# Kernel tuning notes

Hardware: AMD Instinct MI355X
Metric: run time of the kernel (lower is better)

The kernel has to match this reference:

```python
import jax, jax.numpy as jnp
import numpy as np

N_NODES = 40000
N_EDGES = 640000
IN_F = 128
HID = 128
MAX_ITERS = 8  # torch loop runs MAX_ITERS + 1 state updates (epsilon=None)


def setup_inputs() -> dict:
    key = jax.random.key(0)
    k1, k2, k3, k4, k5, k6 = jax.random.split(key, 6)
    x = jax.random.normal(k1, (N_NODES, IN_F), dtype=jnp.float32)
    edge_index = jax.random.randint(k2, (2, N_EDGES), 0, N_NODES, dtype=jnp.int64)
    scale = 0.1 / np.sqrt(HID)  # keep tanh out of deep saturation (ESN-style spectral scaling)
    w_in0 = jax.random.normal(k3, (HID, IN_F), dtype=jnp.float32) * scale   # layer 0 input_weight
    w_rec0 = jax.random.normal(k4, (HID, HID), dtype=jnp.float32) * scale   # layer 0 recurrent_weight
    w_in1 = jax.random.normal(k5, (HID, HID), dtype=jnp.float32) * scale    # layer 1 input_weight
    w_rec1 = jax.random.normal(k6, (HID, HID), dtype=jnp.float32) * scale   # layer 1 recurrent_weight
    return {"edge_index": edge_index, "x": x,
            "w_in0": w_in0, "w_rec0": w_rec0, "w_in1": w_in1, "w_rec1": w_rec1}


def _embed(x_proj, w_rec, src, dst):
    # Fixed-point iteration: state = tanh(x_proj + aggr(state) @ w_rec)
    # aggr = sum of source-node states scattered to destination nodes (PyG aggr='add').
    state0 = jnp.zeros_like(x_proj)

    def step(state, _):
        aggr = jax.ops.segment_sum(state[src], dst, num_segments=N_NODES)  # [N, H]
        new_state = jnp.tanh(x_proj + aggr @ w_rec)
        return new_state, None

    state, _ = jax.lax.scan(step, state0, None, length=MAX_ITERS + 1)
    return state


def reference(edge_index, x, w_in0, w_rec0, w_in1, w_rec1):
    src, dst = edge_index[0], edge_index[1]
    h0 = _embed(x @ w_in0.T, w_rec0, src, dst)    # layer 0 embeddings [N, H]
    h1 = _embed(h0 @ w_in1.T, w_rec1, src, dst)   # layer 1 embeddings [N, H]
    return h1  # fully=False, pooling=None -> final layer node embeddings
```

## Files before the change

### kernel.cpp

```cpp
#include <hip/hip_runtime.h>
#include <math.h>

#define N_NODES 40000
#define N_EDGES 640000
#define HID 128
#define MAXW 64
#define ITERS 8
#define NH (N_NODES * HID)
#define NPB 16
#define FBLK (N_NODES / NPB)
#define DSTRIDE 32

typedef __bf16 bf16x8 __attribute__((ext_vector_type(8)));
typedef __bf16 bf16x4 __attribute__((ext_vector_type(4)));
typedef float floatx4 __attribute__((ext_vector_type(4)));

__global__ __launch_bounds__(256) void init_kernel(int* __restrict__ ell,
                                                   int* __restrict__ degp,
                                                   __bf16* __restrict__ padA,
                                                   __bf16* __restrict__ padB) {
    int i = blockIdx.x * 256 + threadIdx.x;
    int4 pad = {N_NODES, N_NODES, N_NODES, N_NODES};
    ((int4*)ell)[i] = pad;
    if (i < N_NODES * DSTRIDE / 4) {
        int4 z = {0, 0, 0, 0};
        ((int4*)degp)[i] = z;
    }
    if (i < HID / 8) {
        bf16x8 z;
#pragma unroll
        for (int j = 0; j < 8; ++j) z[j] = (__bf16)0.f;
        ((bf16x8*)padA)[i] = z;
        ((bf16x8*)padB)[i] = z;
    }
}

__global__ __launch_bounds__(256) void build_ell_kernel(const int* __restrict__ ei,
                                                        int* __restrict__ degp,
                                                        int* __restrict__ ell) {
    int e = blockIdx.x * 256 + threadIdx.x;
    if (e >= N_EDGES) return;
    int s = ei[e];
    int d = ei[N_EDGES + e];
    int c = atomicAdd(&degp[d * DSTRIDE], 1);
    if (c < MAXW) ell[d * MAXW + c] = s;
}

__global__ __launch_bounds__(256) void compact_deg_kernel(const int* __restrict__ degp,
                                                          int* __restrict__ deg) {
    int i = blockIdx.x * 256 + threadIdx.x;
    if (i >= N_NODES) return;
    int d = degp[i * DSTRIDE];
    deg[i] = d > MAXW ? MAXW : d;
}

__global__ __launch_bounds__(256) void pack_w_kernel(const float* __restrict__ w,
                                                     __bf16* __restrict__ pk, int trans) {
    int f = blockIdx.x * 256 + threadIdx.x;
    int j = f & 7, l = (f >> 3) & 63, t = (f >> 9) & 7, c = f >> 12;
    int k = c * 32 + (l >> 4) * 8 + j;
    int n = t * 16 + (l & 15);
    float v = trans ? w[n * HID + k] : w[k * HID + n];
    pk[f] = (__bf16)v;
}

__global__ __launch_bounds__(256) void cast_bf16_kernel(const float* __restrict__ x,
                                                        __bf16* __restrict__ o) {
    int i = blockIdx.x * 256 + threadIdx.x;
    float4 v = ((const float4*)x)[i];
    bf16x4 b;
    b[0] = (__bf16)v.x; b[1] = (__bf16)v.y; b[2] = (__bf16)v.z; b[3] = (__bf16)v.w;
    ((bf16x4*)o)[i] = b;
}

__global__ __launch_bounds__(256) void mfma_gemm_kernel(const __bf16* A,
                                                        const __bf16* __restrict__ Bpk,
                                                        __bf16* __restrict__ xp_bf,
                                                        __bf16* st_bf) {
    __shared__ float tile[4][16][132];
    int tid = threadIdx.x;
    int wv = tid >> 6, lane = tid & 63;
    int q = lane >> 4, cl = lane & 15;

    int row_a = blockIdx.x * 64 + wv * 16 + cl;
    bf16x8 a[4];
#pragma unroll
    for (int c = 0; c < 4; ++c)
        a[c] = *(const bf16x8*)(A + (size_t)row_a * HID + c * 32 + q * 8);

#pragma unroll
    for (int t = 0; t < 8; ++t) {
        floatx4 acc_t = {0.f, 0.f, 0.f, 0.f};
#pragma unroll
        for (int c = 0; c < 4; ++c) {
            bf16x8 b = *(const bf16x8*)(Bpk + (((c * 8 + t) * 64 + lane) << 3));
            acc_t = __builtin_amdgcn_mfma_f32_16x16x32_bf16(a[c], b, acc_t, 0, 0, 0);
        }
#pragma unroll
        for (int r = 0; r < 4; ++r)
            tile[wv][q * 4 + r][t * 16 + cl] = acc_t[r];
    }
    int row = lane >> 2, seg = lane & 3;
    size_t goff = (size_t)(blockIdx.x * 64 + wv * 16 + row) * HID + seg * 32;
    float v[32];
#pragma unroll
    for (int j = 0; j < 8; ++j) {
        floatx4 t4 = *(floatx4*)&tile[wv][row][seg * 32 + j * 4];
        v[j * 4] = t4[0]; v[j * 4 + 1] = t4[1]; v[j * 4 + 2] = t4[2]; v[j * 4 + 3] = t4[3];
    }
#pragma unroll
    for (int j = 0; j < 4; ++j) {
        bf16x8 o;
#pragma unroll
        for (int k = 0; k < 8; ++k) o[k] = (__bf16)v[j * 8 + k];
        *(bf16x8*)(xp_bf + goff + j * 8) = o;
    }
#pragma unroll
    for (int i = 0; i < 32; ++i) v[i] = tanhf(v[i]);
#pragma unroll
    for (int j = 0; j < 4; ++j) {
        bf16x8 o;
#pragma unroll
        for (int k = 0; k < 8; ++k) o[k] = (__bf16)v[j * 8 + k];
        *(bf16x8*)(st_bf + goff + j * 8) = o;
    }
}

__global__ __launch_bounds__(256, 8) void fused_iter_kernel(
    const __bf16* __restrict__ state_in,
    __bf16* __restrict__ state_out,
    const int* __restrict__ ell,
    const int* __restrict__ deg,
    const __bf16* __restrict__ Bpk,
    const __bf16* __restrict__ xproj,
    float* __restrict__ st_f32) {
    __shared__ __align__(16) char smem[8704];
    int(*ell_lds)[68] = (int(*)[68])smem;
    __bf16(*aggr_lds)[136] = (__bf16(*)[136])(smem + 4352);
    float(*tile)[132] = (float(*)[132])smem;

    int tid = threadIdx.x;
    int wv = tid >> 6, lane = tid & 63;
    int q = lane >> 4, f = lane & 15;
    int nb = blockIdx.x * NPB;

    int degv = deg[nb + (lane & 15)];
    int bmx = degv;
#pragma unroll
    for (int m = 1; m <= 8; m <<= 1) {
        int o = __shfl_xor(bmx, m);
        bmx = o > bmx ? o : bmx;
    }
    int nslots = (bmx + 3) & ~3;

    {
        int n = tid & 15, g = tid >> 4;
        if (g * 4 < nslots)
            *(int4*)&ell_lds[n][g * 4] = *(const int4*)&ell[(size_t)(nb + n) * MAXW + g * 4];
    }
    __syncthreads();

    int n = wv * 4 + q;
    int cn = __shfl(degv, n);
    int steps = (cn + 3) >> 2;
    float acc[8];
#pragma unroll
    for (int j = 0; j < 8; ++j) acc[j] = 0.f;
    for (int s = 0; s < steps; ++s) {
        int b0 = s * 4;
        int idx[4];
#pragma unroll
        for (int u = 0; u < 4; ++u) idx[u] = ell_lds[n][b0 + u];
        bf16x8 v[4];
#pragma unroll
        for (int u = 0; u < 4; ++u)
            v[u] = *(const bf16x8*)(state_in + (size_t)idx[u] * HID + f * 8);
#pragma unroll
        for (int j = 0; j < 8; ++j)
            acc[j] += ((float)v[0][j] + (float)v[1][j]) + ((float)v[2][j] + (float)v[3][j]);
    }
    {
        bf16x8 o;
#pragma unroll
        for (int j = 0; j < 8; ++j) o[j] = (__bf16)acc[j];
        *(bf16x8*)&aggr_lds[n][f * 8] = o;
    }
    __syncthreads();

    bf16x8 a[4];
#pragma unroll
    for (int c = 0; c < 4; ++c)
        a[c] = *(const bf16x8*)&aggr_lds[f][c * 32 + q * 8];
    __syncthreads();

#pragma unroll
    for (int tl = 0; tl < 2; ++tl) {
        int t = wv * 2 + tl;
        floatx4 acc_t = {0.f, 0.f, 0.f, 0.f};
#pragma unroll
        for (int c = 0; c < 4; ++c) {
            bf16x8 b = *(const bf16x8*)(Bpk + (((c * 8 + t) * 64 + lane) << 3));
            acc_t = __builtin_amdgcn_mfma_f32_16x16x32_bf16(a[c], b, acc_t, 0, 0, 0);
        }
#pragma unroll
        for (int r = 0; r < 4; ++r)
            tile[q * 4 + r][t * 16 + f] = acc_t[r];
    }

    int row = lane >> 2, seg = lane & 3;
    size_t goff = (size_t)(nb + row) * HID + wv * 32 + seg * 8;
    int lcol = wv * 32 + seg * 8;
    float v[8];
    bf16x8 bx = *(const bf16x8*)(xproj + goff);
#pragma unroll
    for (int j = 0; j < 2; ++j) {
        floatx4 t4 = *(floatx4*)&tile[row][lcol + j * 4];
        v[j * 4] = t4[0]; v[j * 4 + 1] = t4[1]; v[j * 4 + 2] = t4[2]; v[j * 4 + 3] = t4[3];
    }
#pragma unroll
    for (int k = 0; k < 8; ++k) v[k] = tanhf(v[k] + (float)bx[k]);
    {
        bf16x8 o;
#pragma unroll
        for (int k = 0; k < 8; ++k) o[k] = (__bf16)v[k];
        *(bf16x8*)(state_out + goff) = o;
    }
    if (st_f32) {
#pragma unroll
        for (int j = 0; j < 2; ++j) {
            float4 o = {v[j * 4], v[j * 4 + 1], v[j * 4 + 2], v[j * 4 + 3]};
            *(float4*)(st_f32 + goff + j * 4) = o;
        }
    }
}

extern "C" void kernel_launch(void* const* d_in, const int* in_sizes, int n_in,
                              void* d_out, int out_size, void* d_ws, size_t ws_size,
                              hipStream_t stream) {
    const int* ei = (const int*)d_in[0];
    const float* x = (const float*)d_in[1];
    const float* w_in0 = (const float*)d_in[2];
    const float* w_rec0 = (const float*)d_in[3];
    const float* w_in1 = (const float*)d_in[4];
    const float* w_rec1 = (const float*)d_in[5];
    float* out = (float*)d_out;

    __bf16* xproj_bf = (__bf16*)d_ws;
    __bf16* stateA = xproj_bf + NH;
    __bf16* stateB = stateA + NH + HID;
    __bf16* packs = stateB + NH + HID;
    int* deg = (int*)(packs + 4 * 16384);
    int* degp = deg + N_NODES;
    int* ell = degp + N_NODES * DSTRIDE;
    __bf16* pk_in0 = packs;
    __bf16* pk_rec0 = packs + 16384;
    __bf16* pk_in1 = packs + 2 * 16384;
    __bf16* pk_rec1 = packs + 3 * 16384;

    init_kernel<<<N_EDGES / 256, 256, 0, stream>>>(ell, degp, stateA + NH, stateB + NH);
    build_ell_kernel<<<N_EDGES / 256, 256, 0, stream>>>(ei, degp, ell);
    compact_deg_kernel<<<(N_NODES + 255) / 256, 256, 0, stream>>>(degp, deg);
    pack_w_kernel<<<64, 256, 0, stream>>>(w_in0, pk_in0, 1);
    pack_w_kernel<<<64, 256, 0, stream>>>(w_rec0, pk_rec0, 0);
    pack_w_kernel<<<64, 256, 0, stream>>>(w_in1, pk_in1, 1);
    pack_w_kernel<<<64, 256, 0, stream>>>(w_rec1, pk_rec1, 0);
    cast_bf16_kernel<<<NH / 4 / 256, 256, 0, stream>>>(x, stateB);

    for (int layer = 0; layer < 2; ++layer) {
        const __bf16* pk_in = layer ? pk_in1 : pk_in0;
        const __bf16* pk_rec = layer ? pk_rec1 : pk_rec0;
        const __bf16* xin = layer ? stateA : stateB;
        mfma_gemm_kernel<<<625, 256, 0, stream>>>(xin, pk_in, xproj_bf, stateA);
        for (int it = 0; it < ITERS; ++it) {
            const __bf16* sin = (it & 1) ? stateB : stateA;
            __bf16* sout = (it & 1) ? stateA : stateB;
            float* f32out = (layer == 1 && it == ITERS - 1) ? out : nullptr;
            fused_iter_kernel<<<FBLK, 256, 0, stream>>>(sin, sout, ell, deg,
                                                        pk_rec, xproj_bf, f32out);
        }
    }
}
```

Baseline: 540.6 us.

## Store node state in feature-sliced layout and gather slice by slice

Node state moves from row-major [N,128] to four 32-feature slices, each [N+1,32] with its own zero pad row. The gather loop walks one slice at a time, with four lanes per node covering different neighbours, then reduces across lanes with shuffles. The aim is to shrink the gathered working set per pass so it stays cache-resident, at the cost of extra shuffles and four passes over the neighbour list. Nontemporal loads and stores are added for the ELL indices, xproj and the outputs, and a __syncthreads is added before the tile readback in both kernels.

```diff
diff --git a/kernel.cpp b/kernel.cpp
--- a/kernel.cpp
+++ b/kernel.cpp
@@ -10,10 +10,16 @@
 #define NPB 16
 #define FBLK (N_NODES / NPB)
 #define DSTRIDE 32
+#define NN1 (N_NODES + 1)
+#define SLICES 4
+#define SW 32
 
 typedef __bf16 bf16x8 __attribute__((ext_vector_type(8)));
 typedef __bf16 bf16x4 __attribute__((ext_vector_type(4)));
 typedef float floatx4 __attribute__((ext_vector_type(4)));
+typedef int intx4 __attribute__((ext_vector_type(4)));
+
+union V16 { bf16x8 b; floatx4 f; };
 
 __global__ __launch_bounds__(256) void init_kernel(int* __restrict__ ell,
                                                    int* __restrict__ degp,
@@ -26,12 +32,13 @@
         int4 z = {0, 0, 0, 0};
         ((int4*)degp)[i] = z;
     }
-    if (i < HID / 8) {
+    if (i < 16) {
         bf16x8 z;
 #pragma unroll
         for (int j = 0; j < 8; ++j) z[j] = (__bf16)0.f;
-        ((bf16x8*)padA)[i] = z;
-        ((bf16x8*)padB)[i] = z;
+        size_t off = ((size_t)(i >> 2) * NN1 + N_NODES) * SW + (i & 3) * 8;
+        *(bf16x8*)(padA + off) = z;
+        *(bf16x8*)(padB + off) = z;
     }
 }
 
@@ -70,7 +77,11 @@
     float4 v = ((const float4*)x)[i];
     bf16x4 b;
     b[0] = (__bf16)v.x; b[1] = (__bf16)v.y; b[2] = (__bf16)v.z; b[3] = (__bf16)v.w;
-    ((bf16x4*)o)[i] = b;
+    int node = i >> 5;
+    int r = i & 31;
+    int slice = r >> 3;
+    int within = (r & 7) * 4;
+    *(bf16x4*)(o + ((size_t)slice * NN1 + node) * SW + within) = b;
 }
 
 __global__ __launch_bounds__(256) void mfma_gemm_kernel(const __bf16* A,
@@ -86,7 +97,7 @@
     bf16x8 a[4];
 #pragma unroll
     for (int c = 0; c < 4; ++c)
-        a[c] = *(const bf16x8*)(A + (size_t)row_a * HID + c * 32 + q * 8);
+        a[c] = *(const bf16x8*)(A + ((size_t)c * NN1 + row_a) * SW + q * 8);
 
 #pragma unroll
     for (int t = 0; t < 8; ++t) {
@@ -100,8 +111,10 @@
         for (int r = 0; r < 4; ++r)
             tile[wv][q * 4 + r][t * 16 + cl] = acc_t[r];
     }
+    __syncthreads();
     int row = lane >> 2, seg = lane & 3;
-    size_t goff = (size_t)(blockIdx.x * 64 + wv * 16 + row) * HID + seg * 32;
+    int grow = blockIdx.x * 64 + wv * 16 + row;
+    size_t goff = (size_t)grow * HID + seg * 32;
     float v[32];
 #pragma unroll
     for (int j = 0; j < 8; ++j) {
@@ -122,7 +135,7 @@
         bf16x8 o;
 #pragma unroll
         for (int k = 0; k < 8; ++k) o[k] = (__bf16)v[j * 8 + k];
-        *(bf16x8*)(st_bf + goff + j * 8) = o;
+        *(bf16x8*)(st_bf + ((size_t)seg * NN1 + grow) * SW + j * 8) = o;
     }
 }
 
@@ -144,7 +157,7 @@
     int q = lane >> 4, f = lane & 15;
     int nb = blockIdx.x * NPB;
 
-    int degv = deg[nb + (lane & 15)];
+    int degv = deg[nb + f];
     int bmx = degv;
 #pragma unroll
     for (int m = 1; m <= 8; m <<= 1) {
@@ -155,35 +168,41 @@
 
     {
         int n = tid & 15, g = tid >> 4;
-        if (g * 4 < nslots)
-            *(int4*)&ell_lds[n][g * 4] = *(const int4*)&ell[(size_t)(nb + n) * MAXW + g * 4];
+        if (g * 4 < nslots) {
+            intx4 e4 = __builtin_nontemporal_load(
+                (const intx4*)&ell[(size_t)(nb + n) * MAXW + g * 4]);
+            *(intx4*)&ell_lds[n][g * 4] = e4;
+        }
     }
     __syncthreads();
 
     int n = wv * 4 + q;
     int cn = __shfl(degv, n);
     int steps = (cn + 3) >> 2;
-    float acc[8];
-#pragma unroll
-    for (int j = 0; j < 8; ++j) acc[j] = 0.f;
-    for (int s = 0; s < steps; ++s) {
-        int b0 = s * 4;
-        int idx[4];
-#pragma unroll
-        for (int u = 0; u < 4; ++u) idx[u] = ell_lds[n][b0 + u];
-        bf16x8 v[4];
-#pragma unroll
-        for (int u = 0; u < 4; ++u)
-            v[u] = *(const bf16x8*)(state_in + (size_t)idx[u] * HID + f * 8);
-#pragma unroll
-        for (int j = 0; j < 8; ++j)
-            acc[j] += ((float)v[0][j] + (float)v[1][j]) + ((float)v[2][j] + (float)v[3][j]);
-    }
-    {
-        bf16x8 o;
-#pragma unroll
-        for (int j = 0; j < 8; ++j) o[j] = (__bf16)acc[j];
-        *(bf16x8*)&aggr_lds[n][f * 8] = o;
+    int sub = f >> 2;
+    int fc = f & 3;
+    for (int s = 0; s < SLICES; ++s) {
+        const __bf16* sl = state_in + (size_t)s * NN1 * SW;
+        float acc[8];
+#pragma unroll
+        for (int j = 0; j < 8; ++j) acc[j] = 0.f;
+        for (int st = 0; st < steps; ++st) {
+            int idxm = ell_lds[n][st * 4 + sub];
+            bf16x8 v = *(const bf16x8*)(sl + (size_t)idxm * SW + fc * 8);
+#pragma unroll
+            for (int j = 0; j < 8; ++j) acc[j] += (float)v[j];
+        }
+#pragma unroll
+        for (int j = 0; j < 8; ++j) {
+            acc[j] += __shfl_xor(acc[j], 4);
+            acc[j] += __shfl_xor(acc[j], 8);
+        }
+        if (sub == 0) {
+            bf16x8 o;
+#pragma unroll
+            for (int j = 0; j < 8; ++j) o[j] = (__bf16)acc[j];
+            *(bf16x8*)&aggr_lds[n][s * SW + fc * 8] = o;
+        }
     }
     __syncthreads();
 
@@ -206,12 +225,16 @@
         for (int r = 0; r < 4; ++r)
             tile[q * 4 + r][t * 16 + f] = acc_t[r];
     }
+    __syncthreads();
 
     int row = lane >> 2, seg = lane & 3;
-    size_t goff = (size_t)(nb + row) * HID + wv * 32 + seg * 8;
+    int grow = nb + row;
+    size_t goff = (size_t)grow * HID + wv * 32 + seg * 8;
     int lcol = wv * 32 + seg * 8;
     float v[8];
-    bf16x8 bx = *(const bf16x8*)(xproj + goff);
+    floatx4 bxt = __builtin_nontemporal_load((const floatx4*)(xproj + goff));
+    V16 ubx; ubx.f = bxt;
+    bf16x8 bx = ubx.b;
 #pragma unroll
     for (int j = 0; j < 2; ++j) {
         floatx4 t4 = *(floatx4*)&tile[row][lcol + j * 4];
@@ -223,13 +246,15 @@
         bf16x8 o;
 #pragma unroll
         for (int k = 0; k < 8; ++k) o[k] = (__bf16)v[k];
-        *(bf16x8*)(state_out + goff) = o;
+        V16 uo; uo.b = o;
+        __builtin_nontemporal_store(
+            uo.f, (floatx4*)(state_out + ((size_t)wv * NN1 + grow) * SW + seg * 8));
     }
     if (st_f32) {
 #pragma unroll
         for (int j = 0; j < 2; ++j) {
-            float4 o = {v[j * 4], v[j * 4 + 1], v[j * 4 + 2], v[j * 4 + 3]};
-            *(float4*)(st_f32 + goff + j * 4) = o;
+            floatx4 o = {v[j * 4], v[j * 4 + 1], v[j * 4 + 2], v[j * 4 + 3]};
+            __builtin_nontemporal_store(o, (floatx4*)(st_f32 + goff + j * 4));
         }
     }
 }
@@ -247,8 +272,8 @@
 
     __bf16* xproj_bf = (__bf16*)d_ws;
     __bf16* stateA = xproj_bf + NH;
-    __bf16* stateB = stateA + NH + HID;
-    __bf16* packs = stateB + NH + HID;
+    __bf16* stateB = stateA + (size_t)SLICES * NN1 * SW;
+    __bf16* packs = stateB + (size_t)SLICES * NN1 * SW;
     int* deg = (int*)(packs + 4 * 16384);
     int* degp = deg + N_NODES;
     int* ell = degp + N_NODES * DSTRIDE;
@@ -257,7 +282,7 @@
     __bf16* pk_in1 = packs + 2 * 16384;
     __bf16* pk_rec1 = packs + 3 * 16384;
 
-    init_kernel<<<N_EDGES / 256, 256, 0, stream>>>(ell, degp, stateA + NH, stateB + NH);
+    init_kernel<<<N_EDGES / 256, 256, 0, stream>>>(ell, degp, stateA, stateB);
     build_ell_kernel<<<N_EDGES / 256, 256, 0, stream>>>(ei, degp, ell);
     compact_deg_kernel<<<(N_NODES + 255) / 256, 256, 0, stream>>>(degp, deg);
     pack_w_kernel<<<64, 256, 0, stream>>>(w_in0, pk_in0, 1);
```

Result: slower. 695.2 us (+28.6%).

## Split node state into two feature-half planes and gather each in separate kernels

Applied to the files above, without the earlier changes.

Stores the bf16 node state as two planar halves of 64 features each. Each iteration now runs two kernels: a first kernel gathers and sums neighbours over plane 0 into an aggregate buffer, and the fused kernel gathers plane 1, loads the plane-0 aggregate, then does the MFMA and tanh. The aim is to halve the working set touched by each random gather so that it fits better in cache. The cost is an extra launch and an aggregate round-trip per iteration, plus reading the ELL lists twice; the ELL and xproj loads are also switched to nontemporal.

```diff
diff --git a/kernel.cpp b/kernel.cpp
--- a/kernel.cpp
+++ b/kernel.cpp
@@ -4,6 +4,8 @@
 #define N_NODES 40000
 #define N_EDGES 640000
 #define HID 128
+#define HHID 64
+#define PLANE ((N_NODES + 1) * HHID)
 #define MAXW 64
 #define ITERS 8
 #define NH (N_NODES * HID)
@@ -14,11 +16,14 @@
 typedef __bf16 bf16x8 __attribute__((ext_vector_type(8)));
 typedef __bf16 bf16x4 __attribute__((ext_vector_type(4)));
 typedef float floatx4 __attribute__((ext_vector_type(4)));
+typedef int intx4 __attribute__((ext_vector_type(4)));
+
+union V16 { bf16x8 b; floatx4 f; };
 
 __global__ __launch_bounds__(256) void init_kernel(int* __restrict__ ell,
                                                    int* __restrict__ degp,
-                                                   __bf16* __restrict__ padA,
-                                                   __bf16* __restrict__ padB) {
+                                                   __bf16* __restrict__ stA,
+                                                   __bf16* __restrict__ stB) {
     int i = blockIdx.x * 256 + threadIdx.x;
     int4 pad = {N_NODES, N_NODES, N_NODES, N_NODES};
     ((int4*)ell)[i] = pad;
@@ -26,12 +31,14 @@
         int4 z = {0, 0, 0, 0};
         ((int4*)degp)[i] = z;
     }
-    if (i < HID / 8) {
+    if (i < 8) {
         bf16x8 z;
 #pragma unroll
         for (int j = 0; j < 8; ++j) z[j] = (__bf16)0.f;
-        ((bf16x8*)padA)[i] = z;
-        ((bf16x8*)padB)[i] = z;
+        *(bf16x8*)(stA + (size_t)N_NODES * HHID + i * 8) = z;
+        *(bf16x8*)(stA + PLANE + (size_t)N_NODES * HHID + i * 8) = z;
+        *(bf16x8*)(stB + (size_t)N_NODES * HHID + i * 8) = z;
+        *(bf16x8*)(stB + PLANE + (size_t)N_NODES * HHID + i * 8) = z;
     }
 }
 
@@ -64,19 +71,22 @@
     pk[f] = (__bf16)v;
 }
 
-__global__ __launch_bounds__(256) void cast_bf16_kernel(const float* __restrict__ x,
-                                                        __bf16* __restrict__ o) {
+__global__ __launch_bounds__(256) void cast_planar_kernel(const float* __restrict__ x,
+                                                          __bf16* __restrict__ st) {
     int i = blockIdx.x * 256 + threadIdx.x;
     float4 v = ((const float4*)x)[i];
     bf16x4 b;
     b[0] = (__bf16)v.x; b[1] = (__bf16)v.y; b[2] = (__bf16)v.z; b[3] = (__bf16)v.w;
-    ((bf16x4*)o)[i] = b;
+    int node = i >> 5;
+    int r = i & 31;
+    int plane = r >> 4;
+    *(bf16x4*)(st + (size_t)plane * PLANE + (size_t)node * HHID + (r & 15) * 4) = b;
 }
 
 __global__ __launch_bounds__(256) void mfma_gemm_kernel(const __bf16* A,
                                                         const __bf16* __restrict__ Bpk,
                                                         __bf16* __restrict__ xp_bf,
-                                                        __bf16* st_bf) {
+                                                        __bf16* __restrict__ st) {
     __shared__ float tile[4][16][132];
     int tid = threadIdx.x;
     int wv = tid >> 6, lane = tid & 63;
@@ -86,7 +96,8 @@
     bf16x8 a[4];
 #pragma unroll
     for (int c = 0; c < 4; ++c)
-        a[c] = *(const bf16x8*)(A + (size_t)row_a * HID + c * 32 + q * 8);
+        a[c] = *(const bf16x8*)(A + (size_t)(c >> 1) * PLANE + (size_t)row_a * HHID +
+                                (c & 1) * 32 + q * 8);
 
 #pragma unroll
     for (int t = 0; t < 8; ++t) {
@@ -101,7 +112,8 @@
             tile[wv][q * 4 + r][t * 16 + cl] = acc_t[r];
     }
     int row = lane >> 2, seg = lane & 3;
-    size_t goff = (size_t)(blockIdx.x * 64 + wv * 16 + row) * HID + seg * 32;
+    int grow = blockIdx.x * 64 + wv * 16 + row;
+    size_t goff = (size_t)grow * HID + seg * 32;
     float v[32];
 #pragma unroll
     for (int j = 0; j < 8; ++j) {
@@ -117,22 +129,83 @@
     }
 #pragma unroll
     for (int i = 0; i < 32; ++i) v[i] = tanhf(v[i]);
-#pragma unroll
-    for (int j = 0; j < 4; ++j) {
-        bf16x8 o;
-#pragma unroll
-        for (int k = 0; k < 8; ++k) o[k] = (__bf16)v[j * 8 + k];
-        *(bf16x8*)(st_bf + goff + j * 8) = o;
-    }
-}
-
-__global__ __launch_bounds__(256, 8) void fused_iter_kernel(
+    {
+        __bf16* sb = st + (size_t)(seg >> 1) * PLANE + (size_t)grow * HHID + (seg & 1) * 32;
+#pragma unroll
+        for (int j = 0; j < 4; ++j) {
+            bf16x8 o;
+#pragma unroll
+            for (int k = 0; k < 8; ++k) o[k] = (__bf16)v[j * 8 + k];
+            *(bf16x8*)(sb + j * 8) = o;
+        }
+    }
+}
+
+__global__ __launch_bounds__(256, 8) void gather1_kernel(
+    const __bf16* __restrict__ state_in,
+    __bf16* __restrict__ aggr0,
+    const int* __restrict__ ell,
+    const int* __restrict__ deg) {
+    __shared__ __align__(16) int ell_lds[16][68];
+
+    int tid = threadIdx.x;
+    int wv = tid >> 6, lane = tid & 63;
+    int q = lane >> 4, f = lane & 15;
+    int nb = blockIdx.x * NPB;
+
+    int degv = deg[nb + f];
+    int bmx = degv;
+#pragma unroll
+    for (int m = 1; m <= 8; m <<= 1) {
+        int o = __shfl_xor(bmx, m);
+        bmx = o > bmx ? o : bmx;
+    }
+    int nslots = (bmx + 3) & ~3;
+    {
+        int n = tid & 15, g = tid >> 4;
+        if (g * 4 < nslots) {
+            intx4 e4 = __builtin_nontemporal_load(
+                (const intx4*)&ell[(size_t)(nb + n) * MAXW + g * 4]);
+            *(intx4*)&ell_lds[n][g * 4] = e4;
+        }
+    }
+    __syncthreads();
+
+    int n = wv * 4 + q;
+    int cn = __shfl(degv, n);
+    int steps = (cn + 3) >> 2;
+    float acc[4];
+#pragma unroll
+    for (int j = 0; j < 4; ++j) acc[j] = 0.f;
+    for (int s = 0; s < steps; ++s) {
+        int b0 = s * 4;
+        int idx[4];
+#pragma unroll
+        for (int u = 0; u < 4; ++u) idx[u] = ell_lds[n][b0 + u];
+        bf16x4 v[4];
+#pragma unroll
+        for (int u = 0; u < 4; ++u)
+            v[u] = *(const bf16x4*)(state_in + (size_t)idx[u] * HHID + f * 4);
+#pragma unroll
+        for (int j = 0; j < 4; ++j)
+            acc[j] += ((float)v[0][j] + (float)v[1][j]) + ((float)v[2][j] + (float)v[3][j]);
+    }
+    {
+        bf16x4 o;
+#pragma unroll
+        for (int j = 0; j < 4; ++j) o[j] = (__bf16)acc[j];
+        *(bf16x4*)(aggr0 + (size_t)(nb + n) * HHID + f * 4) = o;
+    }
+}
+
+__global__ __launch_bounds__(256, 8) void fused2_kernel(
     const __bf16* __restrict__ state_in,
     __bf16* __restrict__ state_out,
     const int* __restrict__ ell,
     const int* __restrict__ deg,
     const __bf16* __restrict__ Bpk,
     const __bf16* __restrict__ xproj,
+    const __bf16* __restrict__ aggr0,
     float* __restrict__ st_f32) {
     __shared__ __align__(16) char smem[8704];
     int(*ell_lds)[68] = (int(*)[68])smem;
@@ -144,7 +217,7 @@
     int q = lane >> 4, f = lane & 15;
     int nb = blockIdx.x * NPB;
 
-    int degv = deg[nb + (lane & 15)];
+    int degv = deg[nb + f];
     int bmx = degv;
 #pragma unroll
     for (int m = 1; m <= 8; m <<= 1) {
@@ -152,38 +225,47 @@
         bmx = o > bmx ? o : bmx;
     }
     int nslots = (bmx + 3) & ~3;
-
     {
         int n = tid & 15, g = tid >> 4;
-        if (g * 4 < nslots)
-            *(int4*)&ell_lds[n][g * 4] = *(const int4*)&ell[(size_t)(nb + n) * MAXW + g * 4];
+        if (g * 4 < nslots) {
+            intx4 e4 = __builtin_nontemporal_load(
+                (const intx4*)&ell[(size_t)(nb + n) * MAXW + g * 4]);
+            *(intx4*)&ell_lds[n][g * 4] = e4;
+        }
     }
     __syncthreads();
 
+    {
+        int n = tid >> 4, l = tid & 15;
+        *(bf16x4*)&aggr_lds[n][l * 4] =
+            *(const bf16x4*)(aggr0 + (size_t)(nb + n) * HHID + l * 4);
+    }
+
+    const __bf16* sin1 = state_in + PLANE;
     int n = wv * 4 + q;
     int cn = __shfl(degv, n);
     int steps = (cn + 3) >> 2;
-    float acc[8];
-#pragma unroll
-    for (int j = 0; j < 8; ++j) acc[j] = 0.f;
+    float acc[4];
+#pragma unroll
+    for (int j = 0; j < 4; ++j) acc[j] = 0.f;
     for (int s = 0; s < steps; ++s) {
         int b0 = s * 4;
         int idx[4];
 #pragma unroll
         for (int u = 0; u < 4; ++u) idx[u] = ell_lds[n][b0 + u];
-        bf16x8 v[4];
+        bf16x4 v[4];
 #pragma unroll
         for (int u = 0; u < 4; ++u)
-            v[u] = *(const bf16x8*)(state_in + (size_t)idx[u] * HID + f * 8);
-#pragma unroll
-        for (int j = 0; j < 8; ++j)
+            v[u] = *(const bf16x4*)(sin1 + (size_t)idx[u] * HHID + f * 4);
+#pragma unroll
+        for (int j = 0; j < 4; ++j)
             acc[j] += ((float)v[0][j] + (float)v[1][j]) + ((float)v[2][j] + (float)v[3][j]);
     }
     {
-        bf16x8 o;
-#pragma unroll
-        for (int j = 0; j < 8; ++j) o[j] = (__bf16)acc[j];
-        *(bf16x8*)&aggr_lds[n][f * 8] = o;
+        bf16x4 o;
+#pragma unroll
+        for (int j = 0; j < 4; ++j) o[j] = (__bf16)acc[j];
+        *(bf16x4*)&aggr_lds[n][64 + f * 4] = o;
     }
     __syncthreads();
 
@@ -208,10 +290,13 @@
     }
 
     int row = lane >> 2, seg = lane & 3;
-    size_t goff = (size_t)(nb + row) * HID + wv * 32 + seg * 8;
+    int grow = nb + row;
+    size_t goff = (size_t)grow * HID + wv * 32 + seg * 8;
     int lcol = wv * 32 + seg * 8;
     float v[8];
-    bf16x8 bx = *(const bf16x8*)(xproj + goff);
+    V16 ubx;
+    ubx.f = __builtin_nontemporal_load((const floatx4*)(xproj + goff));
+    bf16x8 bx = ubx.b;
 #pragma unroll
     for (int j = 0; j < 2; ++j) {
         floatx4 t4 = *(floatx4*)&tile[row][lcol + j * 4];
@@ -223,7 +308,8 @@
         bf16x8 o;
 #pragma unroll
         for (int k = 0; k < 8; ++k) o[k] = (__bf16)v[k];
-        *(bf16x8*)(state_out + goff) = o;
+        *(bf16x8*)(state_out + (size_t)(wv >> 1) * PLANE + (size_t)grow * HHID +
+                   (wv & 1) * 32 + seg * 8) = o;
     }
     if (st_f32) {
 #pragma unroll
@@ -247,8 +333,9 @@
 
     __bf16* xproj_bf = (__bf16*)d_ws;
     __bf16* stateA = xproj_bf + NH;
-    __bf16* stateB = stateA + NH + HID;
-    __bf16* packs = stateB + NH + HID;
+    __bf16* stateB = stateA + 2 * PLANE;
+    __bf16* aggr0 = stateB + 2 * PLANE;
+    __bf16* packs = aggr0 + (size_t)N_NODES * HHID;
     int* deg = (int*)(packs + 4 * 16384);
     int* degp = deg + N_NODES;
     int* ell = degp + N_NODES * DSTRIDE;
@@ -257,26 +344,35 @@
     __bf16* pk_in1 = packs + 2 * 16384;
     __bf16* pk_rec1 = packs + 3 * 16384;
 
-    init_kernel<<<N_EDGES / 256, 256, 0, stream>>>(ell, degp, stateA + NH, stateB + NH);
+    init_kernel<<<N_EDGES / 256, 256, 0, stream>>>(ell, degp, stateA, stateB);
     build_ell_kernel<<<N_EDGES / 256, 256, 0, stream>>>(ei, degp, ell);
     compact_deg_kernel<<<(N_NODES + 255) / 256, 256, 0, stream>>>(degp, deg);
     pack_w_kernel<<<64, 256, 0, stream>>>(w_in0, pk_in0, 1);
     pack_w_kernel<<<64, 256, 0, stream>>>(w_rec0, pk_rec0, 0);
     pack_w_kernel<<<64, 256, 0, stream>>>(w_in1, pk_in1, 1);
     pack_w_kernel<<<64, 256, 0, stream>>>(w_rec1, pk_rec1, 0);
-    cast_bf16_kernel<<<NH / 4 / 256, 256, 0, stream>>>(x, stateB);
+    cast_planar_kernel<<<NH / 4 / 256, 256, 0, stream>>>(x, stateA);
 
     for (int layer = 0; layer < 2; ++layer) {
         const __bf16* pk_in = layer ? pk_in1 : pk_in0;
         const __bf16* pk_rec = layer ? pk_rec1 : pk_rec0;
-        const __bf16* xin = layer ? stateA : stateB;
-        mfma_gemm_kernel<<<625, 256, 0, stream>>>(xin, pk_in, xproj_bf, stateA);
+        const __bf16* gin = layer ? stateB : stateA;
+        __bf16* gst = layer ? stateA : stateB;
+        mfma_gemm_kernel<<<625, 256, 0, stream>>>(gin, pk_in, xproj_bf, gst);
         for (int it = 0; it < ITERS; ++it) {
-            const __bf16* sin = (it & 1) ? stateB : stateA;
-            __bf16* sout = (it & 1) ? stateA : stateB;
+            const __bf16* sin;
+            __bf16* sout;
+            if (layer == 0) {
+                sin = (it & 1) ? stateA : stateB;
+                sout = (it & 1) ? stateB : stateA;
+            } else {
+                sin = (it & 1) ? stateB : stateA;
+                sout = (it & 1) ? stateA : stateB;
+            }
             float* f32out = (layer == 1 && it == ITERS - 1) ? out : nullptr;
-            fused_iter_kernel<<<FBLK, 256, 0, stream>>>(sin, sout, ell, deg,
-                                                        pk_rec, xproj_bf, f32out);
-        }
-    }
-}
+            gather1_kernel<<<FBLK, 256, 0, stream>>>(sin, aggr0, ell, deg);
+            fused2_kernel<<<FBLK, 256, 0, stream>>>(sin, sout, ell, deg,
+                                                    pk_rec, xproj_bf, aggr0, f32out);
+        }
+    }
+}
```

After: 685.6 us. 1.27x slower.

## Bucket ELL neighbor lists by source-node range for gather locality

Applied to the files above, without the earlier changes.

Splits each destination's ELL neighbor list into four buckets keyed by source-node range, with per-bucket counts packed into one int. The gather loop walks the buckets in order, so concurrent waves tend to read state rows from the same region of memory, which should improve L2/cache locality. The cost is more padded slots and more loop overhead per bucket. Capping each bucket at 20 entries can silently drop edges when one bucket overflows, even though total degree stays below the old 64 cap.

```diff
diff --git a/kernel.cpp b/kernel.cpp
--- a/kernel.cpp
+++ b/kernel.cpp
@@ -4,12 +4,16 @@
 #define N_NODES 40000
 #define N_EDGES 640000
 #define HID 128
-#define MAXW 64
 #define ITERS 8
 #define NH (N_NODES * HID)
 #define NPB 16
 #define FBLK (N_NODES / NPB)
 #define DSTRIDE 32
+#define BUCK 4
+#define BSLOT 20
+#define ELLW (BUCK * BSLOT)
+#define BRANGE (N_NODES / BUCK)
+#define LBS 24
 
 typedef __bf16 bf16x8 __attribute__((ext_vector_type(8)));
 typedef __bf16 bf16x4 __attribute__((ext_vector_type(4)));
@@ -42,16 +46,23 @@
     if (e >= N_EDGES) return;
     int s = ei[e];
     int d = ei[N_EDGES + e];
-    int c = atomicAdd(&degp[d * DSTRIDE], 1);
-    if (c < MAXW) ell[d * MAXW + c] = s;
+    int p = s / BRANGE;
+    int c = atomicAdd(&degp[d * DSTRIDE + p], 1);
+    if (c < BSLOT) ell[d * ELLW + p * BSLOT + c] = s;
 }
 
 __global__ __launch_bounds__(256) void compact_deg_kernel(const int* __restrict__ degp,
                                                           int* __restrict__ deg) {
     int i = blockIdx.x * 256 + threadIdx.x;
     if (i >= N_NODES) return;
-    int d = degp[i * DSTRIDE];
-    deg[i] = d > MAXW ? MAXW : d;
+    int pk = 0;
+#pragma unroll
+    for (int p = 0; p < BUCK; ++p) {
+        int c = degp[i * DSTRIDE + p];
+        if (c > BSLOT) c = BSLOT;
+        pk |= c << (p * 8);
+    }
+    deg[i] = pk;
 }
 
 __global__ __launch_bounds__(256) void pack_w_kernel(const float* __restrict__ w,
@@ -134,9 +145,9 @@
     const __bf16* __restrict__ Bpk,
     const __bf16* __restrict__ xproj,
     float* __restrict__ st_f32) {
-    __shared__ __align__(16) char smem[8704];
-    int(*ell_lds)[68] = (int(*)[68])smem;
-    __bf16(*aggr_lds)[136] = (__bf16(*)[136])(smem + 4352);
+    __shared__ __align__(16) char smem[10496];
+    int(*ell_lds)[96] = (int(*)[96])smem;
+    __bf16(*aggr_lds)[136] = (__bf16(*)[136])(smem + 6144);
     float(*tile)[132] = (float(*)[132])smem;
 
     int tid = threadIdx.x;
@@ -144,40 +155,54 @@
     int q = lane >> 4, f = lane & 15;
     int nb = blockIdx.x * NPB;
 
-    int degv = deg[nb + (lane & 15)];
-    int bmx = degv;
-#pragma unroll
-    for (int m = 1; m <= 8; m <<= 1) {
-        int o = __shfl_xor(bmx, m);
-        bmx = o > bmx ? o : bmx;
-    }
-    int nslots = (bmx + 3) & ~3;
+    int dpk = deg[nb + f];
+    int ns[BUCK];
+#pragma unroll
+    for (int p = 0; p < BUCK; ++p) {
+        int b = (dpk >> (p * 8)) & 255;
+#pragma unroll
+        for (int m = 1; m <= 8; m <<= 1) {
+            int o = __shfl_xor(b, m);
+            b = o > b ? o : b;
+        }
+        ns[p] = (b + 3) & ~3;
+    }
 
     {
-        int n = tid & 15, g = tid >> 4;
-        if (g * 4 < nslots)
-            *(int4*)&ell_lds[n][g * 4] = *(const int4*)&ell[(size_t)(nb + n) * MAXW + g * 4];
+        int n2 = tid & 15, g = tid >> 4;
+        if (g < 5) {
+#pragma unroll
+            for (int p = 0; p < BUCK; ++p)
+                if (g * 4 < ns[p])
+                    *(int4*)&ell_lds[n2][p * LBS + g * 4] =
+                        *(const int4*)&ell[(size_t)(nb + n2) * ELLW + p * BSLOT + g * 4];
+        }
     }
     __syncthreads();
 
     int n = wv * 4 + q;
-    int cn = __shfl(degv, n);
-    int steps = (cn + 3) >> 2;
+    int cpk = __shfl(dpk, n);
     float acc[8];
 #pragma unroll
     for (int j = 0; j < 8; ++j) acc[j] = 0.f;
-    for (int s = 0; s < steps; ++s) {
-        int b0 = s * 4;
-        int idx[4];
-#pragma unroll
-        for (int u = 0; u < 4; ++u) idx[u] = ell_lds[n][b0 + u];
-        bf16x8 v[4];
-#pragma unroll
-        for (int u = 0; u < 4; ++u)
-            v[u] = *(const bf16x8*)(state_in + (size_t)idx[u] * HID + f * 8);
-#pragma unroll
-        for (int j = 0; j < 8; ++j)
-            acc[j] += ((float)v[0][j] + (float)v[1][j]) + ((float)v[2][j] + (float)v[3][j]);
+#pragma unroll
+    for (int p = 0; p < BUCK; ++p) {
+        int cnt = (cpk >> (p * 8)) & 255;
+        int steps = (cnt + 3) >> 2;
+        const int* eb = &ell_lds[n][p * LBS];
+        for (int s = 0; s < steps; ++s) {
+            int b0 = s * 4;
+            int idx[4];
+#pragma unroll
+            for (int u = 0; u < 4; ++u) idx[u] = eb[b0 + u];
+            bf16x8 v[4];
+#pragma unroll
+            for (int u = 0; u < 4; ++u)
+                v[u] = *(const bf16x8*)(state_in + (size_t)idx[u] * HID + f * 8);
+#pragma unroll
+            for (int j = 0; j < 8; ++j)
+                acc[j] += ((float)v[0][j] + (float)v[1][j]) + ((float)v[2][j] + (float)v[3][j]);
+        }
     }
     {
         bf16x8 o;
@@ -257,7 +282,8 @@
     __bf16* pk_in1 = packs + 2 * 16384;
     __bf16* pk_rec1 = packs + 3 * 16384;
 
-    init_kernel<<<N_EDGES / 256, 256, 0, stream>>>(ell, degp, stateA + NH, stateB + NH);
+    init_kernel<<<N_NODES * ELLW / 4 / 256, 256, 0, stream>>>(ell, degp,
+                                                              stateA + NH, stateB + NH);
     build_ell_kernel<<<N_EDGES / 256, 256, 0, stream>>>(ei, degp, ell);
     compact_deg_kernel<<<(N_NODES + 255) / 256, 256, 0, stream>>>(degp, deg);
     pack_w_kernel<<<64, 256, 0, stream>>>(w_in0, pk_in0, 1);
```

Result: slower. 604.1 us (+11.8%).
